# Kernel tuning notes

Hardware: AMD Instinct MI355X
Metric: run time of the kernel (lower is better)

## Reference

```python
import jax, jax.numpy as jnp
import numpy as np
from jax import lax


def fps(xyz, npoint, init_far):
    # Faithful farthest-point sampling: sequential loop over npoint iterations.
    B, N, _ = xyz.shape
    bidx = jnp.arange(B)

    def step(carry, _):
        dist, far = carry
        c = xyz[bidx, far]                       # (B,3) current centroid
        d = jnp.sum((xyz - c[:, None, :]) ** 2, -1)  # (B,N)
        dist = jnp.minimum(dist, d)
        return (dist, jnp.argmax(dist, -1)), far     # emit index BEFORE update, as in torch

    init = (jnp.full((B, N), 1e10, xyz.dtype), init_far)
    _, cent = lax.scan(step, init, None, length=npoint)  # (npoint, B)
    return cent.T                                         # (B, npoint)


def gather_pts(feat, idx):
    # feat (B,N,C), idx (B,K) -> (B,K,C)
    return jnp.take_along_axis(feat, idx[..., None], axis=1)


def setup_inputs() -> dict:
    key = jax.random.key(0)
    ks = jax.random.split(key, 12)
    B, N = 128, 500

    def w(k, o, i):
        return jax.random.normal(k, (o, i), jnp.float32) * 0.02

    z = lambda o: jnp.zeros((o,), jnp.float32)
    return {
        "x": jax.random.normal(ks[0], (B, N, 3), jnp.float32),
        "conf_W": w(ks[1], 1, 3),   "conf_b": z(1),
        "w1": w(ks[2], 64, 4),      "b1": z(64),
        "w2": w(ks[3], 256, 64),    "b2": z(256),
        "pc1_W": w(ks[4], 256, 256),"pc1_b": z(256),
        "w3": w(ks[5], 256, 259),   "b3": z(256),
        "w4": w(ks[6], 384, 256),   "b4": z(384),
        "pc2_W": w(ks[7], 384, 384),"pc2_b": z(384),
        "w5": w(ks[8], 384, 387),   "b5": z(384),
        "w6": w(ks[9], 512, 384),   "b6": z(512),
        "model_weights": 0,
        "init_far1": jax.random.randint(ks[10], (B,), 0, N),
        "init_far2": jax.random.randint(ks[11], (B,), 0, N),
    }


def reference(x, conf_W, conf_b, w1, b1, w2, b2, pc1_W, pc1_b,
              w3, b3, w4, b4, pc2_W, pc2_b, w5, b5, w6, b6,
              model_weights, init_far1, init_far2):
    relu = jax.nn.relu
    lin = lambda h, W, b: h @ W.T + b

    # ConfidenceScorePredictor: per-point sigmoid score (1 channel)
    conf = jax.nn.sigmoid(lin(x, conf_W, conf_b))            # (B,N,1)
    feat = jnp.concatenate([conf, x], -1)                    # (B,N,4)

    l2 = relu(lin(relu(lin(feat, w1, b1)), w2, b2))          # (B,N,256)
    l3 = lin(l2, pc1_W, pc1_b)                               # Conv1d k=1 == per-point linear

    idx1 = fps(x, 500, init_far1)                            # (B,500)
    nf1 = jnp.concatenate([gather_pts(l3, idx1), gather_pts(x, idx1)], -1)  # (B,500,259)

    l5 = relu(lin(relu(lin(nf1, w3, b3)), w4, b4))           # (B,500,384)
    l6 = lin(l5, pc2_W, pc2_b)                               # (B,500,384)

    idx2 = fps(x, 1000, init_far2)                           # (B,1000), indices < 500
    nf2 = jnp.concatenate([gather_pts(l6, idx2), gather_pts(x, idx2)], -1)  # (B,1000,387)

    l8 = relu(lin(relu(lin(nf2, w5, b5)), w6, b6))           # (B,1000,512)
    return jnp.max(l8, axis=1)                               # MaxPool1d(k=1000) -> (B,512)
```

## Files before the change

### kernel.cpp

```cpp
#include <hip/hip_runtime.h>

typedef unsigned short u16;
typedef short bf16x8 __attribute__((ext_vector_type(8)));
typedef float f32x4 __attribute__((ext_vector_type(4)));
typedef unsigned short us8 __attribute__((ext_vector_type(8)));
typedef unsigned long long u64;

__device__ __forceinline__ float bf2f(u16 u) {
  return __uint_as_float(((unsigned)u) << 16);
}
__device__ __forceinline__ u16 f2bf(float f) {
  unsigned u = __float_as_uint(f);
  u += 0x7fffu + ((u >> 16) & 1u);
  return (u16)(u >> 16);
}
__device__ __forceinline__ float rlf(float v, int l) {
  return __uint_as_float((unsigned)__builtin_amdgcn_readlane(__float_as_int(v), l));
}
__device__ __forceinline__ void gload16(const u16* g, u16* l) {
  __builtin_amdgcn_global_load_lds(
      (const __attribute__((address_space(1))) void*)g,
      (__attribute__((address_space(3))) void*)l, 16, 0, 0);
}

#define M_AB 64000
#define M_C 65536

#define OFF_ARENA_B 49152000u
#define OFF_IDX1 149815296u
#define OFF_FPSD 150071296u
#define OFF_FPSI 150333440u
#define OFF_WB   150583296u

template <int CTRL>
__device__ __forceinline__ float dppmaxf(float v) {
  int s = __builtin_amdgcn_update_dpp(0, __float_as_int(v), CTRL, 0xF, 0xF, true);
  return fmaxf(v, __uint_as_float((unsigned)s));
}

__device__ void fps_seg(const float4* cpt, int* out, const int* init1,
                        float* dstate, int* fstate, int b, int t0, int tcnt,
                        int lane) {
  float px[8], py[8], pz[8], dist[8];
  int base = lane * 8;
#pragma unroll
  for (int j = 0; j < 8; ++j) {
    int p = base + j;
    float4 c = cpt[p < 500 ? p : 0];
    px[j] = c.x; py[j] = c.y; pz[j] = c.z;
  }
  int fidx;
  if (t0 == 0) {
#pragma unroll
    for (int j = 0; j < 8; ++j) dist[j] = 1e10f;
    fidx = init1[b];
  } else {
#pragma unroll
    for (int j = 0; j < 8; ++j) dist[j] = dstate[(b * 64 + lane) * 8 + j];
    fidx = fstate[b];
  }

  int tend = t0 + tcnt;
  for (int t = t0; t < tend; ++t) {
    if (lane == 0) out[t] = fidx;
    if (t == 499) return;
    int lo = fidx >> 3, sl = fidx & 7;
    float cx, cy, cz;
    switch (sl) {
#define FPS_CASE(J) \
  case J: cx = rlf(px[J], lo); cy = rlf(py[J], lo); cz = rlf(pz[J], lo); break;
      FPS_CASE(0) FPS_CASE(1) FPS_CASE(2) FPS_CASE(3)
      FPS_CASE(4) FPS_CASE(5) FPS_CASE(6) FPS_CASE(7)
#undef FPS_CASE
      default: cx = cy = cz = 0.f; break;
    }
#pragma unroll
    for (int j = 0; j < 8; ++j) {
      float dx = __fsub_rn(px[j], cx);
      float dy = __fsub_rn(py[j], cy);
      float dz = __fsub_rn(pz[j], cz);
      float d = __fadd_rn(__fadd_rn(__fmul_rn(dx, dx), __fmul_rn(dy, dy)),
                          __fmul_rn(dz, dz));
      dist[j] = fminf(dist[j], d);
    }
    float m01 = fmaxf(dist[0], dist[1]), m23 = fmaxf(dist[2], dist[3]);
    float m45 = fmaxf(dist[4], dist[5]), m67 = fmaxf(dist[6], dist[7]);
    float lm = fmaxf(fmaxf(m01, m23), fmaxf(m45, m67));
    lm = dppmaxf<0x111>(lm);
    lm = dppmaxf<0x112>(lm);
    lm = dppmaxf<0x114>(lm);
    lm = dppmaxf<0x118>(lm);
    lm = dppmaxf<0x142>(lm);
    lm = dppmaxf<0x143>(lm);
    float mf = rlf(lm, 63);
    int sel = 8;
#pragma unroll
    for (int j = 7; j >= 0; --j) sel = (dist[j] == mf) ? j : sel;
    u64 mask = __ballot(sel != 8);
    int li = (int)__ffsll(mask) - 1;
    int sw = __builtin_amdgcn_readlane(sel, li);
    fidx = li * 8 + sw;
  }
#pragma unroll
  for (int j = 0; j < 8; ++j) dstate[(b * 64 + lane) * 8 + j] = dist[j];
  if (lane == 0) fstate[b] = fidx;
}

#define SMEM_BYTES (16384 * 2 + 1024)

__device__ __forceinline__ void gemm_body(
    const u16* __restrict__ A, int lda, const float* __restrict__ X,
    const int* __restrict__ idx, int mode, const u16* __restrict__ Wb,
    int ldw, const float* __restrict__ bias, u16* __restrict__ C, int ldc,
    int Kp, int N, int act, float* __restrict__ outf, int bx, int by,
    char* smem, int t) {
  u16* lA = (u16*)smem;
  u16* lB = (u16*)(smem + 16384);
  float* red = (float*)(smem + 32768);

  const int m0 = bx * 128, n0 = by * 128;
  const int w = t >> 6, lane = t & 63;
  const int mrow = lane & 15, quad = lane >> 4;
  const int wm = w >> 1, wn = w & 1;

  const int lrow8 = lane >> 3;
  const int sseg = (lane & 7) ^ lrow8;

  const u16* arow[4];
  const u16* wrow[4];
#pragma unroll
  for (int i = 0; i < 4; ++i) {
    int gr = m0 + w * 32 + i * 8 + lrow8;
    if (mode == 0) {
      arow[i] = A + (size_t)gr * lda;
    } else if (mode == 1) {
      int b = gr / 500;
      int p = gr - b * 500;
      int s = idx[b * 500 + p];
      arow[i] = A + ((size_t)b * 500 + s) * lda;
    } else {
      int b = gr >> 9;
      int p = gr & 511;
      arow[i] = A + ((size_t)b * 500 + (p < 500 ? p : 0)) * lda;
    }
    wrow[i] = Wb + (size_t)(n0 + w * 32 + i * 8 + lrow8) * ldw;
  }
  const int fr = t >> 1;
  const int fs0 = (t & 1) * 4;
  const u16* faptr;
  const float* fxptr = nullptr;
  bool fvalid = true;
  {
    int gr = m0 + fr;
    if (mode == 0) {
      faptr = A + (size_t)gr * lda;
    } else if (mode == 1) {
      int b = gr / 500;
      int p = gr - b * 500;
      int s = idx[b * 500 + p];
      size_t sr = (size_t)b * 500 + s;
      faptr = A + sr * lda;
      fxptr = X + sr * 3;
    } else {
      int b = gr >> 9;
      int p = gr & 511;
      fvalid = (p < 500);
      size_t sr = (size_t)b * 500 + (fvalid ? p : 0);
      faptr = A + sr * lda;
      fxptr = X + sr * 3;
    }
  }
  const int kfull = lda & ~63;

  f32x4 acc[4][4];
  const f32x4 fz = {0.f, 0.f, 0.f, 0.f};
#pragma unroll
  for (int i = 0; i < 4; ++i)
#pragma unroll
    for (int j = 0; j < 4; ++j) acc[i][j] = fz;

  for (int k0 = 0; k0 < Kp; k0 += 64) {
    __syncthreads();
#pragma unroll
    for (int i = 0; i < 4; ++i)
      gload16(wrow[i] + k0 + sseg * 8, lB + (w * 32 + i * 8) * 64);
    if (k0 < kfull) {
#pragma unroll
      for (int i = 0; i < 4; ++i)
        gload16(arow[i] + k0 + sseg * 8, lA + (w * 32 + i * 8) * 64);
    } else {
#pragma unroll
      for (int s4 = 0; s4 < 4; ++s4) {
        int seg = fs0 + s4;
        us8 v = {0, 0, 0, 0, 0, 0, 0, 0};
        if (fvalid) {
          int kb = k0 + seg * 8;
#pragma unroll
          for (int j = 0; j < 8; ++j) {
            int k = kb + j;
            u16 vv = 0;
            if (k < lda) vv = faptr[k];
            else if (mode != 0 && k < lda + 3) vv = f2bf(fxptr[k - lda]);
            v[j] = vv;
          }
        }
        *(us8*)(lA + fr * 64 + (seg ^ (fr & 7)) * 8) = v;
      }
    }
    __syncthreads();

#pragma unroll
    for (int kh = 0; kh < 2; ++kh) {
      bf16x8 af[4], bfv[4];
#pragma unroll
      for (int mi = 0; mi < 4; ++mi) {
        int r = wm * 64 + mi * 16 + mrow;
        af[mi] = *(const bf16x8*)(lA + r * 64 + ((kh * 4 + quad) ^ (r & 7)) * 8);
      }
#pragma unroll
      for (int ni = 0; ni < 4; ++ni) {
        int r = wn * 64 + ni * 16 + mrow;
        bfv[ni] = *(const bf16x8*)(lB + r * 64 + ((kh * 4 + quad) ^ (r & 7)) * 8);
      }
#pragma unroll
      for (int mi = 0; mi < 4; ++mi)
#pragma unroll
        for (int ni = 0; ni < 4; ++ni)
          acc[mi][ni] = __builtin_amdgcn_mfma_f32_16x16x32_bf16(
              af[mi], bfv[ni], acc[mi][ni], 0, 0, 0);
    }
  }

  if (act < 2) {
#pragma unroll
    for (int ni = 0; ni < 4; ++ni) {
      int col = n0 + wn * 64 + ni * 16 + mrow;
      if (col >= N) continue;
      float bv = bias[col];
#pragma unroll
      for (int mi = 0; mi < 4; ++mi)
#pragma unroll
        for (int r = 0; r < 4; ++r) {
          int grow = m0 + wm * 64 + mi * 16 + quad * 4 + r;
          float v = acc[mi][ni][r] + bv;
          if (act == 1) v = fmaxf(v, 0.f);
          C[(size_t)grow * ldc + col] = f2bf(v);
        }
    }
  } else {
#pragma unroll
    for (int ni = 0; ni < 4; ++ni) {
      int col = n0 + wn * 64 + ni * 16 + mrow;
      float bv = (col < N) ? bias[col] : 0.f;
      float mx = 0.f;
#pragma unroll
      for (int mi = 0; mi < 4; ++mi)
#pragma unroll
        for (int r = 0; r < 4; ++r) {
          int grow = m0 + wm * 64 + mi * 16 + quad * 4 + r;
          float v = fmaxf(acc[mi][ni][r] + bv, 0.f);
          if ((grow & 511) < 500) mx = fmaxf(mx, v);
        }
      mx = fmaxf(mx, __shfl_xor(mx, 16, 64));
      mx = fmaxf(mx, __shfl_xor(mx, 32, 64));
      if (quad == 0) red[wm * 128 + wn * 64 + ni * 16 + mrow] = mx;
    }
    __syncthreads();
    if (t < 128) {
      int col = n0 + t;
      if (col < N) {
        float m = fmaxf(red[t], red[128 + t]);
        int b = m0 >> 9;
        atomicMax((unsigned*)&outf[b * 512 + col], __float_as_uint(m));
      }
    }
  }
}

__global__ __launch_bounds__(256) void gemm_mfma(
    const u16* __restrict__ A, int lda, const float* __restrict__ X,
    const int* __restrict__ idx, int mode, const u16* __restrict__ Wb,
    int ldw, const float* __restrict__ bias, u16* __restrict__ C, int ldc,
    int Kp, int N, int act, float* __restrict__ outf) {
  __shared__ __align__(16) char smem[SMEM_BYTES];
  gemm_body(A, lda, X, idx, mode, Wb, ldw, bias, C, ldc, Kp, N, act, outf,
            blockIdx.x, blockIdx.y, smem, threadIdx.x);
}

__global__ __launch_bounds__(256) void gemm_fps(
    const u16* __restrict__ A, int lda, const u16* __restrict__ Wb, int ldw,
    const float* __restrict__ bias, u16* __restrict__ C, int ldc, int Kp,
    int N, int act, int gx, const float* __restrict__ x,
    const int* __restrict__ init1, int* __restrict__ idx1,
    float* __restrict__ dstate, int* __restrict__ fstate, int t0, int tcnt) {
  __shared__ __align__(16) char smem[SMEM_BYTES];
  int bid = blockIdx.x;
  int t = threadIdx.x;
  if (bid < 128) {
    int b = bid;
    float4* cpt = (float4*)smem;
    const float* xb = x + (size_t)b * 1500;
    for (int p = t; p < 500; p += 256)
      cpt[p] = make_float4(xb[p * 3], xb[p * 3 + 1], xb[p * 3 + 2], 0.f);
    __syncthreads();
    if (t < 64)
      fps_seg(cpt, idx1 + b * 500, init1, dstate, fstate, b, t0, tcnt, t);
  } else {
    int g = bid - 128;
    int by = g / gx, bx = g - by * gx;
    gemm_body(A, lda, nullptr, nullptr, 0, Wb, ldw, bias, C, ldc, Kp, N, act,
              nullptr, bx, by, smem, t);
  }
}

struct PrepArgs {
  const float* wsrc[8];
  u16* wdst[8];
  int wN[8], wK[8], wKp[8];
  int wstart[9];
};

__global__ __launch_bounds__(256) void prep_kernel(
    PrepArgs pa, const float* __restrict__ x, const float* __restrict__ cW,
    const float* __restrict__ cb, u16* __restrict__ feat,
    float* __restrict__ outf, const int* __restrict__ init1,
    int* __restrict__ idx1, float* __restrict__ dstate,
    int* __restrict__ fstate) {
  __shared__ float4 cpt[512];
  int bid = blockIdx.x;
  int t = threadIdx.x;
  if (bid < 128) {
    int b = bid;
    const float* xb = x + (size_t)b * 1500;
    for (int p = t; p < 500; p += 256)
      cpt[p] = make_float4(xb[p * 3], xb[p * 3 + 1], xb[p * 3 + 2], 0.f);
    __syncthreads();
    if (t < 64) fps_seg(cpt, idx1 + b * 500, init1, dstate, fstate, b, 0, 125, t);
    return;
  }
  int i = (bid - 128) * 256 + t;
  int S = pa.wstart[8];
  if (i < S) {
    int w = 0;
#pragma unroll
    for (int j = 1; j < 8; ++j)
      if (i >= pa.wstart[j]) w = j;
    int local = i - pa.wstart[w];
    int Kp = pa.wKp[w];
    int n = local / Kp, k = local - n * Kp;
    pa.wdst[w][local] =
        (n < pa.wN[w] && k < pa.wK[w]) ? f2bf(pa.wsrc[w][n * pa.wK[w] + k]) : (u16)0;
  } else if (i < S + 65536) {
    outf[i - S] = 0.f;
  } else {
    int r = i - S - 65536;
    if (r < M_AB) {
      float x0 = x[r * 3], x1 = x[r * 3 + 1], x2 = x[r * 3 + 2];
      float z = x0 * cW[0] + x1 * cW[1] + x2 * cW[2] + cb[0];
      float conf = 1.0f / (1.0f + expf(-z));
      feat[r * 4 + 0] = f2bf(conf);
      feat[r * 4 + 1] = f2bf(x0);
      feat[r * 4 + 2] = f2bf(x1);
      feat[r * 4 + 3] = f2bf(x2);
    }
  }
}

extern "C" void kernel_launch(void* const* d_in, const int* in_sizes, int n_in,
                              void* d_out, int out_size, void* d_ws,
                              size_t ws_size, hipStream_t stream) {
  const float* x      = (const float*)d_in[0];
  const float* conf_W = (const float*)d_in[1];
  const float* conf_b = (const float*)d_in[2];
  const float* w1     = (const float*)d_in[3];
  const float* b1     = (const float*)d_in[4];
  const float* w2     = (const float*)d_in[5];
  const float* b2     = (const float*)d_in[6];
  const float* pc1_W  = (const float*)d_in[7];
  const float* pc1_b  = (const float*)d_in[8];
  const float* w3     = (const float*)d_in[9];
  const float* b3     = (const float*)d_in[10];
  const float* w4     = (const float*)d_in[11];
  const float* b4     = (const float*)d_in[12];
  const float* pc2_W  = (const float*)d_in[13];
  const float* pc2_b  = (const float*)d_in[14];
  const float* w5     = (const float*)d_in[15];
  const float* b5     = (const float*)d_in[16];
  const float* w6     = (const float*)d_in[17];
  const float* b6     = (const float*)d_in[18];
  const int* init1    = (const int*)d_in[20];

  char* ws = (char*)d_ws;
  u16* feat = (u16*)(ws + 0);
  u16* l2b  = (u16*)(ws + 0);
  u16* l4b  = (u16*)(ws + 0);
  u16* l6b  = (u16*)(ws + 0);
  u16* l1b  = (u16*)(ws + OFF_ARENA_B);
  u16* l3b  = (u16*)(ws + OFF_ARENA_B);
  u16* l5b  = (u16*)(ws + OFF_ARENA_B);
  u16* l7b  = (u16*)(ws + OFF_ARENA_B);
  int* idx1 = (int*)(ws + OFF_IDX1);
  float* dstate = (float*)(ws + OFF_FPSD);
  int* fstate   = (int*)(ws + OFF_FPSI);
  u16* wb   = (u16*)(ws + OFF_WB);
  float* outf = (float*)d_out;

  PrepArgs pa;
  const float* srcs[8] = {w1, w2, pc1_W, w3, w4, pc2_W, w5, w6};
  int Ns[8]  = {64, 256, 256, 256, 384, 384, 384, 512};
  int Nps[8] = {128, 256, 256, 256, 384, 384, 384, 512};
  int Ks[8]  = {4, 64, 256, 259, 256, 384, 387, 384};
  int Kps[8] = {64, 64, 256, 320, 256, 384, 448, 384};
  u16* WBp[8];
  int cum = 0;
  for (int i = 0; i < 8; ++i) {
    pa.wsrc[i] = srcs[i];
    pa.wdst[i] = WBp[i] = wb + cum;
    pa.wN[i] = Ns[i];
    pa.wK[i] = Ks[i];
    pa.wKp[i] = Kps[i];
    pa.wstart[i] = cum;
    cum += Nps[i] * Kps[i];
  }
  pa.wstart[8] = cum;
  int total = cum + 65536 + M_AB;

  prep_kernel<<<128 + (total + 255) / 256, 256, 0, stream>>>(
      pa, x, conf_W, conf_b, feat, outf, init1, idx1, dstate, fstate);
  gemm_fps<<<128 + 500, 256, 0, stream>>>(feat, 4, WBp[0], 64, b1, l1b, 64,
      64, 64, 1, 500, x, init1, idx1, dstate, fstate, 125, 125);
  gemm_fps<<<128 + 1000, 256, 0, stream>>>(l1b, 64, WBp[1], 64, b2, l2b, 256,
      64, 256, 1, 500, x, init1, idx1, dstate, fstate, 250, 125);
  gemm_fps<<<128 + 1000, 256, 0, stream>>>(l2b, 256, WBp[2], 256, pc1_b, l3b,
      256, 256, 256, 0, 500, x, init1, idx1, dstate, fstate, 375, 125);
  gemm_mfma<<<dim3(500, 2), 256, 0, stream>>>(l3b, 256, x, idx1, 1,
      WBp[3], 320, b3, l4b, 256, 320, 256, 1, nullptr);
  gemm_mfma<<<dim3(500, 3), 256, 0, stream>>>(l4b, 256, nullptr, nullptr, 0,
      WBp[4], 256, b4, l5b, 384, 256, 384, 1, nullptr);
  gemm_mfma<<<dim3(500, 3), 256, 0, stream>>>(l5b, 384, nullptr, nullptr, 0,
      WBp[5], 384, pc2_b, l6b, 384, 384, 384, 0, nullptr);
  gemm_mfma<<<dim3(512, 3), 256, 0, stream>>>(l6b, 384, x, nullptr, 3,
      WBp[6], 448, b5, l7b, 384, 448, 384, 1, nullptr);
  gemm_mfma<<<dim3(512, 4), 256, 0, stream>>>(l7b, 384, nullptr, nullptr, 0,
      WBp[7], 384, b6, nullptr, 0, 384, 512, 2, outf);
}
```

Measured before the change: 473.1 us.

## Defer FPS gather past per-point layers and overlap FPS with more GEMMs

Per-point linear layers commute with a row gather, so layers 3–6 now run on unpermuted points. The idx1 gather moves to the layer-5 input (new mode 4), which pairs each gathered l6 row with the coordinates at the sampled position. This lets the sequential FPS be split across six fused launches with re-tuned step counts, hiding it behind more GEMM work instead of stalling the idx1-dependent GEMM. The FPS inner loop also carries the next centroid's coordinates through readlane from the argmax selection, replacing the per-iteration switch lookup. The trade-off is more FPS segment boundaries, each of which saves and reloads FPS state.

```diff
diff --git a/kernel.cpp b/kernel.cpp
--- a/kernel.cpp
+++ b/kernel.cpp
@@ -59,21 +59,13 @@
     for (int j = 0; j < 8; ++j) dist[j] = dstate[(b * 64 + lane) * 8 + j];
     fidx = fstate[b];
   }
+  float4 c0 = cpt[fidx];
+  float cx = c0.x, cy = c0.y, cz = c0.z;
 
   int tend = t0 + tcnt;
   for (int t = t0; t < tend; ++t) {
     if (lane == 0) out[t] = fidx;
     if (t == 499) return;
-    int lo = fidx >> 3, sl = fidx & 7;
-    float cx, cy, cz;
-    switch (sl) {
-#define FPS_CASE(J) \
-  case J: cx = rlf(px[J], lo); cy = rlf(py[J], lo); cz = rlf(pz[J], lo); break;
-      FPS_CASE(0) FPS_CASE(1) FPS_CASE(2) FPS_CASE(3)
-      FPS_CASE(4) FPS_CASE(5) FPS_CASE(6) FPS_CASE(7)
-#undef FPS_CASE
-      default: cx = cy = cz = 0.f; break;
-    }
 #pragma unroll
     for (int j = 0; j < 8; ++j) {
       float dx = __fsub_rn(px[j], cx);
@@ -94,12 +86,21 @@
     lm = dppmaxf<0x143>(lm);
     float mf = rlf(lm, 63);
     int sel = 8;
-#pragma unroll
-    for (int j = 7; j >= 0; --j) sel = (dist[j] == mf) ? j : sel;
+    float sx = 0.f, sy = 0.f, sz = 0.f;
+#pragma unroll
+    for (int j = 7; j >= 0; --j) {
+      bool hit = (dist[j] == mf);
+      sel = hit ? j : sel;
+      sx = hit ? px[j] : sx;
+      sy = hit ? py[j] : sy;
+      sz = hit ? pz[j] : sz;
+    }
     u64 mask = __ballot(sel != 8);
     int li = (int)__ffsll(mask) - 1;
-    int sw = __builtin_amdgcn_readlane(sel, li);
-    fidx = li * 8 + sw;
+    fidx = li * 8 + __builtin_amdgcn_readlane(sel, li);
+    cx = rlf(sx, li);
+    cy = rlf(sy, li);
+    cz = rlf(sz, li);
   }
 #pragma unroll
   for (int j = 0; j < 8; ++j) dstate[(b * 64 + lane) * 8 + j] = dist[j];
@@ -131,17 +132,14 @@
 #pragma unroll
   for (int i = 0; i < 4; ++i) {
     int gr = m0 + w * 32 + i * 8 + lrow8;
-    if (mode == 0) {
-      arow[i] = A + (size_t)gr * lda;
-    } else if (mode == 1) {
-      int b = gr / 500;
-      int p = gr - b * 500;
-      int s = idx[b * 500 + p];
+    if (mode == 4) {
+      int b = gr >> 9;
+      int p = gr & 511;
+      int pe = (p < 500) ? p : 0;
+      int s = idx[b * 500 + pe];
       arow[i] = A + ((size_t)b * 500 + s) * lda;
     } else {
-      int b = gr >> 9;
-      int p = gr & 511;
-      arow[i] = A + ((size_t)b * 500 + (p < 500 ? p : 0)) * lda;
+      arow[i] = A + (size_t)gr * lda;
     }
     wrow[i] = Wb + (size_t)(n0 + w * 32 + i * 8 + lrow8) * ldw;
   }
@@ -149,25 +147,18 @@
   const int fs0 = (t & 1) * 4;
   const u16* faptr;
   const float* fxptr = nullptr;
-  bool fvalid = true;
   {
     int gr = m0 + fr;
-    if (mode == 0) {
-      faptr = A + (size_t)gr * lda;
-    } else if (mode == 1) {
-      int b = gr / 500;
-      int p = gr - b * 500;
-      int s = idx[b * 500 + p];
-      size_t sr = (size_t)b * 500 + s;
-      faptr = A + sr * lda;
-      fxptr = X + sr * 3;
-    } else {
+    if (mode == 4) {
       int b = gr >> 9;
       int p = gr & 511;
-      fvalid = (p < 500);
-      size_t sr = (size_t)b * 500 + (fvalid ? p : 0);
-      faptr = A + sr * lda;
-      fxptr = X + sr * 3;
+      int pe = (p < 500) ? p : 0;
+      int s = idx[b * 500 + pe];
+      faptr = A + ((size_t)b * 500 + s) * lda;
+      fxptr = X + ((size_t)b * 500 + pe) * 3;
+    } else {
+      faptr = A + (size_t)gr * lda;
+      if (mode == 2) fxptr = X + (size_t)gr * 3;
     }
   }
   const int kfull = lda & ~63;
@@ -193,16 +184,14 @@
       for (int s4 = 0; s4 < 4; ++s4) {
         int seg = fs0 + s4;
         us8 v = {0, 0, 0, 0, 0, 0, 0, 0};
-        if (fvalid) {
-          int kb = k0 + seg * 8;
-#pragma unroll
-          for (int j = 0; j < 8; ++j) {
-            int k = kb + j;
-            u16 vv = 0;
-            if (k < lda) vv = faptr[k];
-            else if (mode != 0 && k < lda + 3) vv = f2bf(fxptr[k - lda]);
-            v[j] = vv;
-          }
+        int kb = k0 + seg * 8;
+#pragma unroll
+        for (int j = 0; j < 8; ++j) {
+          int k = kb + j;
+          u16 vv = 0;
+          if (k < lda) vv = faptr[k];
+          else if (mode != 0 && k < lda + 3) vv = f2bf(fxptr[k - lda]);
+          v[j] = vv;
         }
         *(us8*)(lA + fr * 64 + (seg ^ (fr & 7)) * 8) = v;
       }
@@ -288,7 +277,8 @@
 }
 
 __global__ __launch_bounds__(256) void gemm_fps(
-    const u16* __restrict__ A, int lda, const u16* __restrict__ Wb, int ldw,
+    const u16* __restrict__ A, int lda, const float* __restrict__ X,
+    int mode, const u16* __restrict__ Wb, int ldw,
     const float* __restrict__ bias, u16* __restrict__ C, int ldc, int Kp,
     int N, int act, int gx, const float* __restrict__ x,
     const int* __restrict__ init1, int* __restrict__ idx1,
@@ -308,7 +298,7 @@
   } else {
     int g = bid - 128;
     int by = g / gx, bx = g - by * gx;
-    gemm_body(A, lda, nullptr, nullptr, 0, Wb, ldw, bias, C, ldc, Kp, N, act,
+    gemm_body(A, lda, X, nullptr, mode, Wb, ldw, bias, C, ldc, Kp, N, act,
               nullptr, bx, by, smem, t);
   }
 }
@@ -325,7 +315,7 @@
     const float* __restrict__ cb, u16* __restrict__ feat,
     float* __restrict__ outf, const int* __restrict__ init1,
     int* __restrict__ idx1, float* __restrict__ dstate,
-    int* __restrict__ fstate) {
+    int* __restrict__ fstate, int tcnt) {
   __shared__ float4 cpt[512];
   int bid = blockIdx.x;
   int t = threadIdx.x;
@@ -335,7 +325,7 @@
     for (int p = t; p < 500; p += 256)
       cpt[p] = make_float4(xb[p * 3], xb[p * 3 + 1], xb[p * 3 + 2], 0.f);
     __syncthreads();
-    if (t < 64) fps_seg(cpt, idx1 + b * 500, init1, dstate, fstate, b, 0, 125, t);
+    if (t < 64) fps_seg(cpt, idx1 + b * 500, init1, dstate, fstate, b, 0, tcnt, t);
     return;
   }
   int i = (bid - 128) * 256 + t;
@@ -394,7 +384,7 @@
   u16* feat = (u16*)(ws + 0);
   u16* l2b  = (u16*)(ws + 0);
   u16* l4b  = (u16*)(ws + 0);
-  u16* l6b  = (u16*)(ws + 0);
+  u16* l6u  = (u16*)(ws + 0);
   u16* l1b  = (u16*)(ws + OFF_ARENA_B);
   u16* l3b  = (u16*)(ws + OFF_ARENA_B);
   u16* l5b  = (u16*)(ws + OFF_ARENA_B);
@@ -426,20 +416,20 @@
   int total = cum + 65536 + M_AB;
 
   prep_kernel<<<128 + (total + 255) / 256, 256, 0, stream>>>(
-      pa, x, conf_W, conf_b, feat, outf, init1, idx1, dstate, fstate);
-  gemm_fps<<<128 + 500, 256, 0, stream>>>(feat, 4, WBp[0], 64, b1, l1b, 64,
-      64, 64, 1, 500, x, init1, idx1, dstate, fstate, 125, 125);
-  gemm_fps<<<128 + 1000, 256, 0, stream>>>(l1b, 64, WBp[1], 64, b2, l2b, 256,
-      64, 256, 1, 500, x, init1, idx1, dstate, fstate, 250, 125);
-  gemm_fps<<<128 + 1000, 256, 0, stream>>>(l2b, 256, WBp[2], 256, pc1_b, l3b,
-      256, 256, 256, 0, 500, x, init1, idx1, dstate, fstate, 375, 125);
-  gemm_mfma<<<dim3(500, 2), 256, 0, stream>>>(l3b, 256, x, idx1, 1,
-      WBp[3], 320, b3, l4b, 256, 320, 256, 1, nullptr);
-  gemm_mfma<<<dim3(500, 3), 256, 0, stream>>>(l4b, 256, nullptr, nullptr, 0,
-      WBp[4], 256, b4, l5b, 384, 256, 384, 1, nullptr);
-  gemm_mfma<<<dim3(500, 3), 256, 0, stream>>>(l5b, 384, nullptr, nullptr, 0,
-      WBp[5], 384, pc2_b, l6b, 384, 384, 384, 0, nullptr);
-  gemm_mfma<<<dim3(512, 3), 256, 0, stream>>>(l6b, 384, x, nullptr, 3,
+      pa, x, conf_W, conf_b, feat, outf, init1, idx1, dstate, fstate, 60);
+  gemm_fps<<<128 + 500, 256, 0, stream>>>(feat, 4, nullptr, 0, WBp[0], 64,
+      b1, l1b, 64, 64, 64, 1, 500, x, init1, idx1, dstate, fstate, 60, 40);
+  gemm_fps<<<128 + 1000, 256, 0, stream>>>(l1b, 64, nullptr, 0, WBp[1], 64,
+      b2, l2b, 256, 64, 256, 1, 500, x, init1, idx1, dstate, fstate, 100, 50);
+  gemm_fps<<<128 + 1000, 256, 0, stream>>>(l2b, 256, nullptr, 0, WBp[2], 256,
+      pc1_b, l3b, 256, 256, 256, 0, 500, x, init1, idx1, dstate, fstate, 150, 70);
+  gemm_fps<<<128 + 1000, 256, 0, stream>>>(l3b, 256, x, 2, WBp[3], 320,
+      b3, l4b, 256, 320, 256, 1, 500, x, init1, idx1, dstate, fstate, 220, 85);
+  gemm_fps<<<128 + 1500, 256, 0, stream>>>(l4b, 256, nullptr, 0, WBp[4], 256,
+      b4, l5b, 384, 256, 384, 1, 500, x, init1, idx1, dstate, fstate, 305, 90);
+  gemm_fps<<<128 + 1500, 256, 0, stream>>>(l5b, 384, nullptr, 0, WBp[5], 384,
+      pc2_b, l6u, 384, 384, 384, 0, 500, x, init1, idx1, dstate, fstate, 395, 105);
+  gemm_mfma<<<dim3(512, 3), 256, 0, stream>>>(l6u, 384, x, idx1, 4,
       WBp[6], 448, b5, l7b, 384, 448, 384, 1, nullptr);
   gemm_mfma<<<dim3(512, 4), 256, 0, stream>>>(l7b, 384, nullptr, nullptr, 0,
       WBp[7], 384, b6, nullptr, 0, 384, 512, 2, outf);
```

Result: faster. 400.0 us (-15.4%).
